# Performance work log

Measured on AMD Instinct MI355X. Metric: run time of the kernel, lower is better.

Reference implementation:

```python
import jax, jax.numpy as jnp
import numpy as np

N_NODES = 50000
N_EDGES = 600000
FEAT = 128
HIDDEN = 128
N_LAYERS = 3


def setup_inputs() -> dict:
    key = jax.random.key(0)
    ks = jax.random.split(key, 6)
    x = jax.random.normal(ks[0], (N_NODES, FEAT), dtype=jnp.float32)
    edge_index = jax.random.randint(ks[1], (2, N_EDGES), 0, N_NODES, dtype=jnp.int32)
    s_in = 1.0 / np.sqrt(FEAT)
    s_h = 1.0 / np.sqrt(HIDDEN)
    W_in = jax.random.uniform(ks[2], (FEAT, HIDDEN), dtype=jnp.float32, minval=-s_in, maxval=s_in)
    b_in = jax.random.uniform(ks[3], (HIDDEN,), dtype=jnp.float32, minval=-s_in, maxval=s_in)
    W_layers = jax.random.uniform(ks[4], (N_LAYERS, HIDDEN, HIDDEN), dtype=jnp.float32, minval=-s_h, maxval=s_h)
    b_layers = jax.random.uniform(ks[5], (N_LAYERS, HIDDEN), dtype=jnp.float32, minval=-s_h, maxval=s_h)
    return {"x": x, "edge_index": edge_index, "W_in": W_in, "b_in": b_in,
            "W_layers": W_layers, "b_layers": b_layers}


def reference(x, edge_index, W_in, b_in, W_layers, b_layers):
    n = x.shape[0]
    # GCNConv: add self-loops, symmetric normalization D^-1/2 (A+I) D^-1/2
    loop = jnp.arange(n, dtype=edge_index.dtype)
    src = jnp.concatenate([edge_index[0], loop])  # [E+N]
    dst = jnp.concatenate([edge_index[1], loop])  # [E+N]
    deg = jax.ops.segment_sum(jnp.ones_like(dst, dtype=x.dtype), dst, num_segments=n)
    inv_sqrt = jnp.where(deg > 0, jax.lax.rsqrt(jnp.maximum(deg, 1e-12)), 0.0)
    coeff = (inv_sqrt[src] * inv_sqrt[dst])[:, None]  # [E+N, 1]

    h = x @ W_in + b_in  # [N, H]
    for l in range(W_layers.shape[0]):
        m = h @ W_layers[l]                       # transform first (GCNConv)
        msgs = m[src] * coeff                     # gather + normalize, [E+N, H]
        agg = jax.ops.segment_sum(msgs, dst, num_segments=n) + b_layers[l]
        h = jax.nn.gelu(agg, approximate=False) + h  # exact GELU + residual
    return h
```

## Files before the change

kernel.cpp:

```cpp
#include <hip/hip_runtime.h>
#include <hip/hip_bf16.h>
#include <math.h>

#define NN 50000
#define NE 600000
#define HD 128
#define NL 3
#define NBLK 49
#define TW_BLKS 64
#define GB 782
#define NCHUNK 512
#define CHK 1172
#define FIL_BLKS (8 * NCHUNK)
#define DRANGE 6250
#define ISQ_BLKS 196
#define ELLW 64
#define ZERO_OFF (NN << 8)

typedef __attribute__((ext_vector_type(8))) short short8;
typedef __attribute__((ext_vector_type(4))) float f32x4;

__device__ __forceinline__ ushort f2bf(float v) {
    union { float f; unsigned u; } c; c.f = v;
    unsigned u = c.u;
    u = (u + 0x7fffu + ((u >> 16) & 1u)) >> 16;
    return (ushort)u;
}
__device__ __forceinline__ float u2f(uint u) {
    union { uint u; float f; } c; c.u = u; return c.f;
}

__global__ __launch_bounds__(256) void init_k(int* __restrict__ cnt,
                                              const float* __restrict__ W_in,
                                              const float* __restrict__ W_layers,
                                              ushort* __restrict__ WT,
                                              ushort* __restrict__ mh) {
    int b = blockIdx.x;
    if (b < NBLK) {
        int base = b * 1024 + threadIdx.x * 4;
        if (base + 4 <= NN) {
            *(int4*)(cnt + base) = int4{0, 0, 0, 0};
        } else {
            for (int u = 0; u < 4; ++u) if (base + u < NN) cnt[base + u] = 0;
        }
        if (b == 0 && threadIdx.x < 64)
            ((uint*)(mh + (size_t)NN * HD))[threadIdx.x] = 0u;
    } else {
        int tloc = (b - NBLK) * 256 + threadIdx.x;
        #pragma unroll
        for (int q = 0; q < 4; ++q) {
            int idx = tloc + q * 16384;
            int m = idx >> 14;
            int c = (idx >> 7) & 127;
            int k = idx & 127;
            const float* W = (m == 0) ? W_in : (W_layers + (size_t)(m - 1) * HD * HD);
            WT[idx] = f2bf(W[k * HD + c]);
        }
    }
}

template<int MODE>
__device__ __forceinline__ void gemm_body(int bid, const void* __restrict__ Av,
                                          const ushort* __restrict__ WT,
                                          const float* __restrict__ bs,
                                          ushort* __restrict__ out_b16,
                                          int nrows, ushort* swT) {
    int tid = threadIdx.x;
    #pragma unroll
    for (int i = 0; i < 8; ++i) {
        int chunk = tid + i * 256;
        int lin = chunk << 4;
        int n = lin >> 8;
        int swz = lin ^ ((n & 7) << 4);
        *(float4*)((char*)swT + swz) = *(const float4*)(WT + chunk * 8);
    }
    __syncthreads();

    int w = tid >> 6, l = tid & 63;
    int ar = l & 15, ag = l >> 4;
    int r0 = bid * 64 + w * 16;
    int arow = r0 + ar;
    bool arow_ok = arow < nrows;

    short8 afr[4];
    #pragma unroll
    for (int ks = 0; ks < 4; ++ks) {
        if (MODE == 0) {
            short8 fr = {0,0,0,0,0,0,0,0};
            if (arow_ok) {
                const float* Af = (const float*)Av;
                float4 p0 = *(const float4*)(Af + (size_t)arow * HD + ks * 32 + ag * 8);
                float4 p1 = *(const float4*)(Af + (size_t)arow * HD + ks * 32 + ag * 8 + 4);
                fr[0] = (short)f2bf(p0.x); fr[1] = (short)f2bf(p0.y);
                fr[2] = (short)f2bf(p0.z); fr[3] = (short)f2bf(p0.w);
                fr[4] = (short)f2bf(p1.x); fr[5] = (short)f2bf(p1.y);
                fr[6] = (short)f2bf(p1.z); fr[7] = (short)f2bf(p1.w);
            }
            afr[ks] = fr;
        } else {
            const ushort* Ab = (const ushort*)Av;
            afr[ks] = arow_ok ? *(const short8*)(Ab + (size_t)arow * HD + ks * 32 + ag * 8)
                              : short8{0,0,0,0,0,0,0,0};
        }
    }

    f32x4 acc[8];
    #pragma unroll
    for (int t = 0; t < 8; ++t) acc[t] = f32x4{0.f, 0.f, 0.f, 0.f};

    #pragma unroll
    for (int ks = 0; ks < 4; ++ks) {
        #pragma unroll
        for (int t = 0; t < 8; ++t) {
            int n = t * 16 + ar;
            int lin = (n << 8) + ks * 64 + ag * 16;
            int swz = lin ^ ((ar & 7) << 4);
            short8 b = *(const short8*)((const char*)swT + swz);
            acc[t] = __builtin_amdgcn_mfma_f32_16x16x32_bf16(afr[ks], b, acc[t], 0, 0, 0);
        }
    }

    #pragma unroll
    for (int q = 0; q < 4; ++q) {
        int row = r0 + ag * 4 + q;
        if (row >= nrows) continue;
        if (MODE == 0) {
            #pragma unroll
            for (int t = 0; t < 8; ++t) {
                int col = t * 16 + ar;
                out_b16[(size_t)row * HD + col] = f2bf(acc[t][q] + bs[col]);
            }
        } else {
            float s = bs[row];
            #pragma unroll
            for (int t = 0; t < 8; ++t) {
                int col = t * 16 + ar;
                out_b16[(size_t)row * HD + col] = f2bf(acc[t][q] * s);
            }
        }
    }
}

__global__ __launch_bounds__(256) void gemm0_ell_k(const float* __restrict__ x,
                                                   const ushort* __restrict__ WT,
                                                   const float* __restrict__ b_in,
                                                   ushort* __restrict__ hb,
                                                   const int* __restrict__ src,
                                                   const int* __restrict__ dst,
                                                   int* __restrict__ cnt,
                                                   int* __restrict__ ell) {
    __shared__ ushort swT[HD * HD];
    int b = blockIdx.x;
    if (b < GB) {
        gemm_body<0>(b, x, WT, b_in, hb, NN, swT);
        return;
    }
    int r = b & 7;
    int j = (b - GB) >> 3;
    int dlo = r * DRANGE, dhi = dlo + DRANGE;
    int base = j * CHK;
    int end = min(base + CHK, NE);
    for (int e = base + (int)threadIdx.x; e < end; e += 256) {
        int d = dst[e];
        if (d >= dlo && d < dhi) {
            int pos = atomicAdd(&cnt[d], 1);
            if (pos < ELLW) ell[(d << 6) + pos] = src[e] << 8;
        }
    }
}

__global__ __launch_bounds__(256) void gemm1_isq_k(const ushort* __restrict__ hb,
                                                   const ushort* __restrict__ WT1,
                                                   const float* __restrict__ dummy_isq,
                                                   ushort* __restrict__ mh,
                                                   const int* __restrict__ cnt,
                                                   float* __restrict__ isq) {
    __shared__ ushort swT[HD * HD];
    int b = blockIdx.x;
    if (b < GB) {
        gemm_body<1>(b, hb, WT1, dummy_isq, mh, NN, swT);
        return;
    }
    int v = (b - GB) * 256 + threadIdx.x;
    if (v < NN) isq[v] = rsqrtf((float)(cnt[v] + 1));
}


__global__ __launch_bounds__(256) void gemm_mfma_k(const ushort* __restrict__ A,
                                                   const ushort* __restrict__ WT,
                                                   const float* __restrict__ isq,
                                                   ushort* __restrict__ mh) {
    __shared__ ushort swT[HD * HD];
    gemm_body<1>(blockIdx.x, A, WT, isq, mh, NN, swT);
}

__global__ __launch_bounds__(256) void isq_k(const int* __restrict__ cnt,
                                             float* __restrict__ isq) {
    int v = blockIdx.x * 256 + threadIdx.x;
    if (v < NN) isq[v] = rsqrtf((float)(cnt[v] + 1));
}

template<int LAST>
__global__ __launch_bounds__(256) void aggregate_k(const ushort* __restrict__ mh,
                                                   const int* __restrict__ cntp,
                                                   const int* __restrict__ ell,
                                                   const float* __restrict__ isq,
                                                   const float* __restrict__ bias,
                                                   float* __restrict__ h,
                                                   ushort* __restrict__ hb) {
    int gw = (int)((blockIdx.x * blockDim.x + threadIdx.x) >> 6);
    int lane = threadIdx.x & 63;
    if (gw >= NN) return;
    int v = gw;
    int cnt = min(cntp[v], ELLW);
    const char* mh_lane = (const char*)mh + lane * 4;

    uint sp = *(const uint*)(mh_lane + ((size_t)v << 8));
    float accx = u2f(sp << 16), accy = u2f(sp & 0xffff0000u);

    int offs = (lane < cnt) ? ell[(v << 6) + lane] : ZERO_OFF;
    int nb = (cnt + 15) >> 4;
    for (int b = 0; b < nb; ++b) {
        int jb = b << 4;
        int o0  = __shfl(offs, jb);
        int o1  = __shfl(offs, jb + 1);
        int o2  = __shfl(offs, jb + 2);
        int o3  = __shfl(offs, jb + 3);
        int o4  = __shfl(offs, jb + 4);
        int o5  = __shfl(offs, jb + 5);
        int o6  = __shfl(offs, jb + 6);
        int o7  = __shfl(offs, jb + 7);
        int o8  = __shfl(offs, jb + 8);
        int o9  = __shfl(offs, jb + 9);
        int o10 = __shfl(offs, jb + 10);
        int o11 = __shfl(offs, jb + 11);
        int o12 = __shfl(offs, jb + 12);
        int o13 = __shfl(offs, jb + 13);
        int o14 = __shfl(offs, jb + 14);
        int o15 = __shfl(offs, jb + 15);
        uint p0  = *(const uint*)(mh_lane + o0);
        uint p1  = *(const uint*)(mh_lane + o1);
        uint p2  = *(const uint*)(mh_lane + o2);
        uint p3  = *(const uint*)(mh_lane + o3);
        uint p4  = *(const uint*)(mh_lane + o4);
        uint p5  = *(const uint*)(mh_lane + o5);
        uint p6  = *(const uint*)(mh_lane + o6);
        uint p7  = *(const uint*)(mh_lane + o7);
        uint p8  = *(const uint*)(mh_lane + o8);
        uint p9  = *(const uint*)(mh_lane + o9);
        uint p10 = *(const uint*)(mh_lane + o10);
        uint p11 = *(const uint*)(mh_lane + o11);
        uint p12 = *(const uint*)(mh_lane + o12);
        uint p13 = *(const uint*)(mh_lane + o13);
        uint p14 = *(const uint*)(mh_lane + o14);
        uint p15 = *(const uint*)(mh_lane + o15);
        accx += u2f(p0 << 16);  accy += u2f(p0 & 0xffff0000u);
        accx += u2f(p1 << 16);  accy += u2f(p1 & 0xffff0000u);
        accx += u2f(p2 << 16);  accy += u2f(p2 & 0xffff0000u);
        accx += u2f(p3 << 16);  accy += u2f(p3 & 0xffff0000u);
        accx += u2f(p4 << 16);  accy += u2f(p4 & 0xffff0000u);
        accx += u2f(p5 << 16);  accy += u2f(p5 & 0xffff0000u);
        accx += u2f(p6 << 16);  accy += u2f(p6 & 0xffff0000u);
        accx += u2f(p7 << 16);  accy += u2f(p7 & 0xffff0000u);
        accx += u2f(p8 << 16);  accy += u2f(p8 & 0xffff0000u);
        accx += u2f(p9 << 16);  accy += u2f(p9 & 0xffff0000u);
        accx += u2f(p10 << 16); accy += u2f(p10 & 0xffff0000u);
        accx += u2f(p11 << 16); accy += u2f(p11 & 0xffff0000u);
        accx += u2f(p12 << 16); accy += u2f(p12 & 0xffff0000u);
        accx += u2f(p13 << 16); accy += u2f(p13 & 0xffff0000u);
        accx += u2f(p14 << 16); accy += u2f(p14 & 0xffff0000u);
        accx += u2f(p15 << 16); accy += u2f(p15 & 0xffff0000u);
    }

    float is = isq[v];
    float2 b = *(const float2*)&bias[lane * 2];
    float ax = accx * is + b.x;
    float ay = accy * is + b.y;
    float gx = 0.5f * ax * (1.f + erff(ax * 0.70710678118654752f));
    float gy = 0.5f * ay * (1.f + erff(ay * 0.70710678118654752f));
    uint* hbp = (uint*)((char*)hb + ((size_t)v << 8) + lane * 4);
    uint hp0 = *hbp;
    float hx = u2f(hp0 << 16) + gx;
    float hy = u2f(hp0 & 0xffff0000u) + gy;
    if (LAST) {
        *(float2*)(h + (size_t)v * HD + lane * 2) = float2{hx, hy};
    } else {
        *hbp = ((uint)f2bf(hx)) | (((uint)f2bf(hy)) << 16);
    }
}


static inline size_t align_up(size_t x, size_t a) { return (x + a - 1) & ~(a - 1); }

extern "C" void kernel_launch(void* const* d_in, const int* in_sizes, int n_in,
                              void* d_out, int out_size, void* d_ws, size_t ws_size,
                              hipStream_t stream) {
    const float* x        = (const float*)d_in[0];
    const int*   eidx     = (const int*)d_in[1];
    const float* W_in     = (const float*)d_in[2];
    const float* b_in     = (const float*)d_in[3];
    const float* W_layers = (const float*)d_in[4];
    const float* b_layers = (const float*)d_in[5];
    float* h = (float*)d_out;

    const int* src = eidx;
    const int* dst = eidx + NE;

    char* p = (char*)d_ws;
    ushort* mh = (ushort*)p;      p += align_up(sizeof(ushort) * ((size_t)NN + 1) * HD, 256);
    ushort* hb = (ushort*)p;      p += align_up(sizeof(ushort) * (size_t)NN * HD, 256);
    ushort* WT = (ushort*)p;      p += align_up(sizeof(ushort) * 4 * HD * HD, 256);
    float* isq = (float*)p;       p += align_up(sizeof(float) * NN, 256);
    int* cnt = (int*)p;           p += align_up(sizeof(int) * NN, 256);
    int* ell = (int*)p;           p += align_up(sizeof(int) * (size_t)NN * ELLW, 256);

    init_k<<<NBLK + TW_BLKS, 256, 0, stream>>>(cnt, W_in, W_layers, WT, mh);
    gemm0_ell_k<<<GB + FIL_BLKS, 256, 0, stream>>>(x, WT, b_in, hb, src, dst, cnt, ell);
    isq_k<<<ISQ_BLKS, 256, 0, stream>>>(cnt, isq);

    for (int l = 0; l < NL; ++l) {
        gemm_mfma_k<<<GB, 256, 0, stream>>>(hb, WT + (size_t)(l + 1) * HD * HD,
                                            isq, mh);
        if (l < NL - 1)
            aggregate_k<0><<<(NN + 3) / 4, 256, 0, stream>>>(mh, cnt, ell, isq,
                                                             b_layers + (size_t)l * HD, h, hb);
        else
            aggregate_k<1><<<(NN + 3) / 4, 256, 0, stream>>>(mh, cnt, ell, isq,
                                                             b_layers + (size_t)l * HD, h, hb);
    }
}
```

Baseline: 172.9 us.

## Build ELL adjacency via LDS histogram and scan instead of global atomics

Replaces the global-atomic ELL construction with a two-pass counting sort. A per-block LDS histogram over destination ranges is followed by a column scan that produces offsets, degree counts and the inverse sqrt degree. A fill pass then places edges using LDS atomics. The fill pass is fused into the first layer's GEMM launch, which removes the separate isq kernel and the count zeroing. The cost is an extra pass over dst and a large histogram scratch buffer, and slot order within each row now follows block order rather than atomic arrival.

```diff
diff --git a/kernel.cpp b/kernel.cpp
--- a/kernel.cpp
+++ b/kernel.cpp
@@ -6,14 +6,13 @@
 #define NE 600000
 #define HD 128
 #define NL 3
-#define NBLK 49
 #define TW_BLKS 64
 #define GB 782
-#define NCHUNK 512
-#define CHK 1172
-#define FIL_BLKS (8 * NCHUNK)
+#define NRES 8
+#define BPR 32
+#define PBLK (NRES * BPR)
+#define ECHUNK 18750
 #define DRANGE 6250
-#define ISQ_BLKS 196
 #define ELLW 64
 #define ZERO_OFF (NN << 8)
 
@@ -30,32 +29,25 @@
     union { uint u; float f; } c; c.u = u; return c.f;
 }
 
-__global__ __launch_bounds__(256) void init_k(int* __restrict__ cnt,
-                                              const float* __restrict__ W_in,
+__global__ __launch_bounds__(256) void init_k(const float* __restrict__ W_in,
                                               const float* __restrict__ W_layers,
                                               ushort* __restrict__ WT,
                                               ushort* __restrict__ mh) {
     int b = blockIdx.x;
-    if (b < NBLK) {
-        int base = b * 1024 + threadIdx.x * 4;
-        if (base + 4 <= NN) {
-            *(int4*)(cnt + base) = int4{0, 0, 0, 0};
-        } else {
-            for (int u = 0; u < 4; ++u) if (base + u < NN) cnt[base + u] = 0;
-        }
-        if (b == 0 && threadIdx.x < 64)
+    if (b == 0) {
+        if (threadIdx.x < 64)
             ((uint*)(mh + (size_t)NN * HD))[threadIdx.x] = 0u;
-    } else {
-        int tloc = (b - NBLK) * 256 + threadIdx.x;
-        #pragma unroll
-        for (int q = 0; q < 4; ++q) {
-            int idx = tloc + q * 16384;
-            int m = idx >> 14;
-            int c = (idx >> 7) & 127;
-            int k = idx & 127;
-            const float* W = (m == 0) ? W_in : (W_layers + (size_t)(m - 1) * HD * HD);
-            WT[idx] = f2bf(W[k * HD + c]);
-        }
+        return;
+    }
+    int tloc = (b - 1) * 256 + threadIdx.x;
+    #pragma unroll
+    for (int q = 0; q < 4; ++q) {
+        int idx = tloc + q * 16384;
+        int m = idx >> 14;
+        int c = (idx >> 7) & 127;
+        int k = idx & 127;
+        const float* W = (m == 0) ? W_in : (W_layers + (size_t)(m - 1) * HD * HD);
+        WT[idx] = f2bf(W[k * HD + c]);
     }
 }
 
@@ -141,50 +133,84 @@
     }
 }
 
-__global__ __launch_bounds__(256) void gemm0_ell_k(const float* __restrict__ x,
-                                                   const ushort* __restrict__ WT,
-                                                   const float* __restrict__ b_in,
-                                                   ushort* __restrict__ hb,
-                                                   const int* __restrict__ src,
-                                                   const int* __restrict__ dst,
-                                                   int* __restrict__ cnt,
-                                                   int* __restrict__ ell) {
+__global__ __launch_bounds__(256) void gemm0_hist_k(const float* __restrict__ x,
+                                                    const ushort* __restrict__ WT,
+                                                    const float* __restrict__ b_in,
+                                                    ushort* __restrict__ hb,
+                                                    const int* __restrict__ dst,
+                                                    int* __restrict__ hist) {
     __shared__ ushort swT[HD * HD];
-    int b = blockIdx.x;
-    if (b < GB) {
-        gemm_body<0>(b, x, WT, b_in, hb, NN, swT);
+    int blk = blockIdx.x;
+    if (blk < GB) {
+        gemm_body<0>(blk, x, WT, b_in, hb, NN, swT);
         return;
     }
-    int r = b & 7;
-    int j = (b - GB) >> 3;
-    int dlo = r * DRANGE, dhi = dlo + DRANGE;
-    int base = j * CHK;
-    int end = min(base + CHK, NE);
+    int p = blk - GB;
+    int r = p & 7, b = p >> 3;
+    int dlo = r * DRANGE;
+    int* lh = (int*)swT;
+    for (int i = threadIdx.x; i < DRANGE; i += 256) lh[i] = 0;
+    __syncthreads();
+    int base = b * ECHUNK, end = min(base + ECHUNK, NE);
     for (int e = base + (int)threadIdx.x; e < end; e += 256) {
-        int d = dst[e];
-        if (d >= dlo && d < dhi) {
-            int pos = atomicAdd(&cnt[d], 1);
-            if (pos < ELLW) ell[(d << 6) + pos] = src[e] << 8;
-        }
-    }
-}
-
-__global__ __launch_bounds__(256) void gemm1_isq_k(const ushort* __restrict__ hb,
-                                                   const ushort* __restrict__ WT1,
-                                                   const float* __restrict__ dummy_isq,
-                                                   ushort* __restrict__ mh,
-                                                   const int* __restrict__ cnt,
-                                                   float* __restrict__ isq) {
+        int d = dst[e] - dlo;
+        if ((unsigned)d < DRANGE) atomicAdd(&lh[d], 1);
+    }
+    __syncthreads();
+    int* hp = hist + (size_t)p * DRANGE;
+    for (int i = threadIdx.x; i < DRANGE; i += 256) hp[i] = lh[i];
+}
+
+__global__ __launch_bounds__(256) void scan_isq_k(int* __restrict__ hist,
+                                                  int* __restrict__ cnt,
+                                                  float* __restrict__ isq) {
+    int r = blockIdx.x & 7;
+    int d = (blockIdx.x >> 3) * 256 + threadIdx.x;
+    if (d >= DRANGE) return;
+    int run = 0;
+    #pragma unroll 4
+    for (int b = 0; b < BPR; ++b) {
+        size_t idx = (size_t)((b << 3) | r) * DRANGE + d;
+        int c = hist[idx];
+        hist[idx] = run;
+        run += c;
+    }
+    int v = r * DRANGE + d;
+    cnt[v] = run;
+    isq[v] = rsqrtf((float)(run + 1));
+}
+
+__global__ __launch_bounds__(256) void gemm1_fill_k(const ushort* __restrict__ hb,
+                                                    const ushort* __restrict__ WT1,
+                                                    const float* __restrict__ isq,
+                                                    ushort* __restrict__ mh,
+                                                    const int* __restrict__ src,
+                                                    const int* __restrict__ dst,
+                                                    const int* __restrict__ hist,
+                                                    int* __restrict__ ell) {
     __shared__ ushort swT[HD * HD];
-    int b = blockIdx.x;
-    if (b < GB) {
-        gemm_body<1>(b, hb, WT1, dummy_isq, mh, NN, swT);
+    int blk = blockIdx.x;
+    if (blk < GB) {
+        gemm_body<1>(blk, hb, WT1, isq, mh, NN, swT);
         return;
     }
-    int v = (b - GB) * 256 + threadIdx.x;
-    if (v < NN) isq[v] = rsqrtf((float)(cnt[v] + 1));
-}
-
+    int p = blk - GB;
+    int r = p & 7, b = p >> 3;
+    int dlo = r * DRANGE;
+    int* lc = (int*)swT;
+    const int* hp = hist + (size_t)p * DRANGE;
+    for (int i = threadIdx.x; i < DRANGE; i += 256) lc[i] = hp[i];
+    __syncthreads();
+    int base = b * ECHUNK, end = min(base + ECHUNK, NE);
+    for (int e = base + (int)threadIdx.x; e < end; e += 256) {
+        int d = dst[e] - dlo;
+        if ((unsigned)d < DRANGE) {
+            int slot = atomicAdd(&lc[d], 1);
+            if (slot < ELLW)
+                ell[((size_t)(d + dlo) << 6) + slot] = src[e] << 8;
+        }
+    }
+}
 
 __global__ __launch_bounds__(256) void gemm_mfma_k(const ushort* __restrict__ A,
                                                    const ushort* __restrict__ WT,
@@ -192,12 +218,6 @@
                                                    ushort* __restrict__ mh) {
     __shared__ ushort swT[HD * HD];
     gemm_body<1>(blockIdx.x, A, WT, isq, mh, NN, swT);
-}
-
-__global__ __launch_bounds__(256) void isq_k(const int* __restrict__ cnt,
-                                             float* __restrict__ isq) {
-    int v = blockIdx.x * 256 + threadIdx.x;
-    if (v < NN) isq[v] = rsqrtf((float)(cnt[v] + 1));
 }
 
 template<int LAST>
@@ -313,14 +333,19 @@
     float* isq = (float*)p;       p += align_up(sizeof(float) * NN, 256);
     int* cnt = (int*)p;           p += align_up(sizeof(int) * NN, 256);
     int* ell = (int*)p;           p += align_up(sizeof(int) * (size_t)NN * ELLW, 256);
-
-    init_k<<<NBLK + TW_BLKS, 256, 0, stream>>>(cnt, W_in, W_layers, WT, mh);
-    gemm0_ell_k<<<GB + FIL_BLKS, 256, 0, stream>>>(x, WT, b_in, hb, src, dst, cnt, ell);
-    isq_k<<<ISQ_BLKS, 256, 0, stream>>>(cnt, isq);
+    int* hist = (int*)p;          p += align_up(sizeof(int) * (size_t)PBLK * DRANGE, 256);
+
+    init_k<<<1 + TW_BLKS, 256, 0, stream>>>(W_in, W_layers, WT, mh);
+    gemm0_hist_k<<<GB + PBLK, 256, 0, stream>>>(x, WT, b_in, hb, dst, hist);
+    scan_isq_k<<<8 * ((DRANGE + 255) / 256), 256, 0, stream>>>(hist, cnt, isq);
+    gemm1_fill_k<<<GB + PBLK, 256, 0, stream>>>(hb, WT + (size_t)HD * HD, isq, mh,
+                                                src, dst, hist, ell);
 
     for (int l = 0; l < NL; ++l) {
-        gemm_mfma_k<<<GB, 256, 0, stream>>>(hb, WT + (size_t)(l + 1) * HD * HD,
-                                            isq, mh);
+        if (l > 0) {
+            gemm_mfma_k<<<GB, 256, 0, stream>>>(hb, WT + (size_t)(l + 1) * HD * HD,
+                                                isq, mh);
+        }
         if (l < NL - 1)
             aggregate_k<0><<<(NN + 3) / 4, 256, 0, stream>>>(mh, cnt, ell, isq,
                                                              b_layers + (size_t)l * HD, h, hb);
```

Result: slower. 217.2 us (+25.6%).
